# Kernel optimization log

Hardware: AMD Instinct MI355X
Metric: run time of the kernel (lower is better)

## Reference

```python
import jax, jax.numpy as jnp
import numpy as np

N = 8192
HIDDEN = 1024
PROJ = 128
T = 0.07
LN_EPS = 1e-12


def _neg_indices(n):
    # Static [n, n-2] index matrix: for row i, all j except j==i and the
    # paired sample j == (i + n//2) % n. Computed with numpy (n is static).
    half = n // 2
    idx = np.arange(n)
    mask = np.ones((n, n), dtype=bool)
    mask[idx, idx] = False
    mask[idx, (idx + half) % n] = False
    return np.nonzero(mask)[1].reshape(n, n - 2)


def setup_inputs() -> dict:
    key = jax.random.key(0)
    ks = jax.random.split(key, 3)
    scale = 1.0 / np.sqrt(HIDDEN)
    return {
        "x": jax.random.normal(ks[0], (N, HIDDEN), dtype=jnp.float32),
        "dense_w": jax.random.normal(ks[1], (HIDDEN, HIDDEN), dtype=jnp.float32) * scale,
        "dense_b": jnp.zeros((HIDDEN,), dtype=jnp.float32),
        "ln_gamma": jnp.ones((HIDDEN,), dtype=jnp.float32),
        "ln_beta": jnp.zeros((HIDDEN,), dtype=jnp.float32),
        "dec_w": jax.random.normal(ks[2], (HIDDEN, PROJ), dtype=jnp.float32) * scale,
        "dec_b": jnp.zeros((PROJ,), dtype=jnp.float32),
    }


def reference(x, dense_w, dense_b, ln_gamma, ln_beta, dec_w, dec_b):
    # dense -> gelu (exact, erf-based as in BERT) -> layernorm -> decoder
    h = x @ dense_w + dense_b
    h = jax.nn.gelu(h, approximate=False)
    mu = jnp.mean(h, axis=-1, keepdims=True)
    var = jnp.mean(jnp.square(h - mu), axis=-1, keepdims=True)
    h = (h - mu) * jax.lax.rsqrt(var + LN_EPS) * ln_gamma + ln_beta
    z = h @ dec_w + dec_b  # [N, 128]

    n = z.shape[0]
    half = n // 2
    # positive logit: dot(z_i, z_partner)
    l_pos = jnp.sum(z[:half] * z[half:], axis=-1)  # [N/2]
    l_pos = jnp.concatenate([l_pos, l_pos])[:, None]  # [N, 1]

    # full similarity matrix, then gather the N-2 negatives per row
    sims = z @ z.T  # [N, N]
    neg_idx = jnp.asarray(_neg_indices(n))  # static [N, N-2]
    l_neg = jnp.take_along_axis(sims, neg_idx, axis=1)  # [N, N-2]

    logits = jnp.concatenate([l_pos, l_neg], axis=1) / T  # [N, N-1]
    # CrossEntropyLoss with labels == 0
    loss = jnp.mean(jax.nn.logsumexp(logits, axis=-1) - logits[:, 0])
    return loss
```

## Files before the change

kernel.cpp:

```cpp
#include <hip/hip_runtime.h>
#include <math.h>
#include <stdint.h>

#define NN 8192
#define HID 1024
#define PROJ 128

constexpr float INV_T = 1.0f / 0.07f;
constexpr float LN_EPS = 1e-12f;
constexpr float CC = 14.285714285714286f * 1.4426950408889634f;

typedef __bf16 bf16x8 __attribute__((ext_vector_type(8)));
typedef float f32x4 __attribute__((ext_vector_type(4)));

#define EXP2(x) __builtin_amdgcn_exp2f(x)

#define GLD16(g, l)                                                     \
  __builtin_amdgcn_global_load_lds(                                     \
      (const __attribute__((address_space(1))) uint32_t*)(g),           \
      (__attribute__((address_space(3))) uint32_t*)(l), 16, 0, 0)

__device__ __forceinline__ uint16_t f2bf(float f) {
  union { float f; uint32_t u; } c; c.f = f;
  uint32_t r = (c.u + 0x7FFFu + ((c.u >> 16) & 1u)) >> 16;
  return (uint16_t)r;
}
__device__ __forceinline__ float bf2f(uint16_t u) {
  union { uint32_t u; float f; } c; c.u = ((uint32_t)u) << 16;
  return c.f;
}

__global__ __launch_bounds__(256) void k_conv(const float* __restrict__ in,
                                              uint16_t* __restrict__ out) {
  int i = (blockIdx.x * 256 + threadIdx.x) * 4;
  float4 v = *(const float4*)(in + i);
  ushort4 o;
  o.x = f2bf(v.x); o.y = f2bf(v.y); o.z = f2bf(v.z); o.w = f2bf(v.w);
  *(ushort4*)(out + i) = o;
}

__global__ __launch_bounds__(256) void k_transpose(const float* __restrict__ in,
                                                   uint16_t* __restrict__ out,
                                                   int R, int C) {
  __shared__ uint16_t t[32][33];
  const int cb = blockIdx.x * 32, rb = blockIdx.y * 32;
  const int tr = threadIdx.x >> 3, tc4 = (threadIdx.x & 7) * 4;
  float4 v = *(const float4*)(in + (size_t)(rb + tr) * C + cb + tc4);
  t[tc4 + 0][tr] = f2bf(v.x);
  t[tc4 + 1][tr] = f2bf(v.y);
  t[tc4 + 2][tr] = f2bf(v.z);
  t[tc4 + 3][tr] = f2bf(v.w);
  __syncthreads();
  const int oc = threadIdx.x >> 3, or4 = (threadIdx.x & 7) * 4;
  ushort4 o;
  o.x = t[oc][or4 + 0]; o.y = t[oc][or4 + 1];
  o.z = t[oc][or4 + 2]; o.w = t[oc][or4 + 3];
  *(ushort4*)(out + (size_t)(cb + oc) * R + rb + or4) = o;
}

__global__ __launch_bounds__(256) void k_gemm1(
    const uint16_t* __restrict__ Ab, const uint16_t* __restrict__ Bt,
    const float* __restrict__ bias, uint16_t* __restrict__ Hout) {
  __shared__ __align__(16) uint16_t As[128 * 32];
  __shared__ __align__(16) uint16_t Bs[128 * 32];
  const int tid = threadIdx.x;
  const int bn = blockIdx.x * 128, bm = blockIdx.y * 128;
  const int wave = tid >> 6, lane = tid & 63;
  const int wx = wave & 1, wy = wave >> 1;
  const int col = lane & 15, quad = lane >> 4;
  f32x4 acc[4][4] = {};
  const char* Abase = (const char*)Ab;
  const char* Bbase = (const char*)Bt;
  for (int k0 = 0; k0 < HID; k0 += 32) {
    __syncthreads();
#pragma unroll
    for (int l = 0; l < 2; ++l) {
      int off = tid * 16 + l * 4096;
      int row = off >> 6, inner = off & 63;
      GLD16(Abase + ((size_t)(bm + row) * HID + k0) * 2 + inner,
            (char*)As + off);
    }
#pragma unroll
    for (int l = 0; l < 2; ++l) {
      int off = tid * 16 + l * 4096;
      int row = off >> 6, inner = off & 63;
      GLD16(Bbase + ((size_t)(bn + row) * HID + k0) * 2 + inner,
            (char*)Bs + off);
    }
    __syncthreads();
    bf16x8 a[4], b[4];
#pragma unroll
    for (int mt = 0; mt < 4; ++mt)
      a[mt] = *(const bf16x8*)&As[(wy * 64 + mt * 16 + col) * 32 + quad * 8];
#pragma unroll
    for (int nt = 0; nt < 4; ++nt)
      b[nt] = *(const bf16x8*)&Bs[(wx * 64 + nt * 16 + col) * 32 + quad * 8];
#pragma unroll
    for (int mt = 0; mt < 4; ++mt)
#pragma unroll
      for (int nt = 0; nt < 4; ++nt)
        acc[mt][nt] = __builtin_amdgcn_mfma_f32_16x16x32_bf16(
            a[mt], b[nt], acc[mt][nt], 0, 0, 0);
  }
  const float is2 = 0.70710678118654752f;
#pragma unroll
  for (int nt = 0; nt < 4; ++nt) {
    int gj = bn + wx * 64 + nt * 16 + col;
    float bv = bias[gj];
#pragma unroll
    for (int mt = 0; mt < 4; ++mt) {
#pragma unroll
      for (int r = 0; r < 4; ++r) {
        int gi = bm + wy * 64 + mt * 16 + quad * 4 + r;
        float v = acc[mt][nt][r] + bv;
        float g = 0.5f * v * (1.0f + erff(v * is2));
        Hout[(size_t)gi * HID + gj] = f2bf(g);
      }
    }
  }
}

__global__ __launch_bounds__(256) void k_layernorm(
    uint16_t* __restrict__ Hm, const float* __restrict__ gamma,
    const float* __restrict__ beta) {
  const int row = blockIdx.x;
  const int tid = threadIdx.x;
  uint16_t* hr = Hm + (size_t)row * HID;
  ushort4 u = *(const ushort4*)(hr + tid * 4);
  float f0 = bf2f(u.x), f1 = bf2f(u.y), f2 = bf2f(u.z), f3 = bf2f(u.w);
  float sum = f0 + f1 + f2 + f3;
  float sq = f0 * f0 + f1 * f1 + f2 * f2 + f3 * f3;
#pragma unroll
  for (int off = 32; off > 0; off >>= 1) {
    sum += __shfl_down(sum, off);
    sq += __shfl_down(sq, off);
  }
  __shared__ float rs[4], rq[4];
  __shared__ float mu_s, rstd_s;
  const int wave = tid >> 6, lane = tid & 63;
  if (lane == 0) { rs[wave] = sum; rq[wave] = sq; }
  __syncthreads();
  if (tid == 0) {
    float s = rs[0] + rs[1] + rs[2] + rs[3];
    float q = rq[0] + rq[1] + rq[2] + rq[3];
    float mu = s * (1.0f / HID);
    float var = q * (1.0f / HID) - mu * mu;
    mu_s = mu;
    rstd_s = rsqrtf(var + LN_EPS);
  }
  __syncthreads();
  const float mu = mu_s, r = rstd_s;
  float4 g = *(const float4*)(gamma + tid * 4);
  float4 b = *(const float4*)(beta + tid * 4);
  ushort4 o;
  o.x = f2bf((f0 - mu) * r * g.x + b.x);
  o.y = f2bf((f1 - mu) * r * g.y + b.y);
  o.z = f2bf((f2 - mu) * r * g.z + b.z);
  o.w = f2bf((f3 - mu) * r * g.w + b.w);
  *(ushort4*)(hr + tid * 4) = o;
}

__global__ __launch_bounds__(256) void k_gemm2(
    const uint16_t* __restrict__ Hn, const uint16_t* __restrict__ Wt2,
    const float* __restrict__ bd, uint16_t* __restrict__ Z) {
  __shared__ __align__(16) uint16_t As2[64 * 32];
  __shared__ __align__(16) uint16_t Bs2[128 * 32];
  const int tid = threadIdx.x;
  const int bm = blockIdx.x * 64;
  const int wave = tid >> 6, lane = tid & 63;
  const int wx = wave & 1, wy = wave >> 1;
  const int col = lane & 15, quad = lane >> 4;
  f32x4 acc[2][4] = {};
  const char* Abase = (const char*)Hn;
  const char* Bbase = (const char*)Wt2;
  for (int k0 = 0; k0 < HID; k0 += 32) {
    __syncthreads();
    {
      int off = tid * 16;
      int row = off >> 6, inner = off & 63;
      GLD16(Abase + ((size_t)(bm + row) * HID + k0) * 2 + inner,
            (char*)As2 + off);
    }
#pragma unroll
    for (int l = 0; l < 2; ++l) {
      int off = tid * 16 + l * 4096;
      int row = off >> 6, inner = off & 63;
      GLD16(Bbase + ((size_t)row * HID + k0) * 2 + inner, (char*)Bs2 + off);
    }
    __syncthreads();
    bf16x8 a[2], b[4];
#pragma unroll
    for (int mt = 0; mt < 2; ++mt)
      a[mt] = *(const bf16x8*)&As2[(wy * 32 + mt * 16 + col) * 32 + quad * 8];
#pragma unroll
    for (int nt = 0; nt < 4; ++nt)
      b[nt] = *(const bf16x8*)&Bs2[(wx * 64 + nt * 16 + col) * 32 + quad * 8];
#pragma unroll
    for (int mt = 0; mt < 2; ++mt)
#pragma unroll
      for (int nt = 0; nt < 4; ++nt)
        acc[mt][nt] = __builtin_amdgcn_mfma_f32_16x16x32_bf16(
            a[mt], b[nt], acc[mt][nt], 0, 0, 0);
  }
#pragma unroll
  for (int nt = 0; nt < 4; ++nt) {
    int gj = wx * 64 + nt * 16 + col;
    float bv = bd[gj];
#pragma unroll
    for (int mt = 0; mt < 2; ++mt)
#pragma unroll
      for (int r = 0; r < 4; ++r) {
        int gi = bm + wy * 32 + mt * 16 + quad * 4 + r;
        Z[(size_t)gi * PROJ + gj] = f2bf(acc[mt][nt][r] + bv);
      }
  }
}

__device__ __forceinline__ void lse_update(float& m, float& s, float v0,
                                           float v1, float v2, float v3) {
  float lm = fmaxf(fmaxf(v0, v1), fmaxf(v2, v3));
  float mn = fmaxf(m, lm);
  float t = mn * CC;
  s = s * EXP2(m * CC - t) + EXP2(v0 * CC - t) + EXP2(v1 * CC - t) +
      EXP2(v2 * CC - t) + EXP2(v3 * CC - t);
  m = mn;
}

__global__ __launch_bounds__(256) void k_sim(const uint16_t* __restrict__ Z,
                                             float* __restrict__ m_part,
                                             float* __restrict__ s_part,
                                             float* __restrict__ pos_arr) {
  __shared__ __align__(16) uint16_t Zi[128 * 136];
  __shared__ __align__(16) uint16_t Zj[128 * 136];
  const int tid = threadIdx.x;
  const int bi = blockIdx.x * 128;
  const int chunk = blockIdx.y;
  const int wave = tid >> 6, lane = tid & 63;
  const int wx = wave & 1, wy = wave >> 1;
  const int col = lane & 15, quad = lane >> 4;

#pragma unroll
  for (int l = 0; l < 8; ++l) {
    int idx = tid + l * 256;
    int row = idx >> 4, kq = (idx & 15) * 8;
    *(uint4*)&Zi[row * 136 + kq] = *(const uint4*)(Z + (size_t)(bi + row) * PROJ + kq);
  }
  float mrow[16], srow[16];
#pragma unroll
  for (int i = 0; i < 16; ++i) { mrow[i] = -INFINITY; srow[i] = 0.f; }

  const int jbase = chunk * 1024;
  for (int t = 0; t < 8; ++t) {
    const int j0 = jbase + t * 128;
    __syncthreads();
#pragma unroll
    for (int l = 0; l < 8; ++l) {
      int idx = tid + l * 256;
      int row = idx >> 4, kq = (idx & 15) * 8;
      *(uint4*)&Zj[row * 136 + kq] =
          *(const uint4*)(Z + (size_t)(j0 + row) * PROJ + kq);
    }
    __syncthreads();
    f32x4 acc[4][4] = {};
#pragma unroll
    for (int kc = 0; kc < 4; ++kc) {
      bf16x8 a[4], b[4];
#pragma unroll
      for (int mt = 0; mt < 4; ++mt)
        a[mt] = *(const bf16x8*)&Zi[(wy * 64 + mt * 16 + col) * 136 +
                                    kc * 32 + quad * 8];
#pragma unroll
      for (int nt = 0; nt < 4; ++nt)
        b[nt] = *(const bf16x8*)&Zj[(wx * 64 + nt * 16 + col) * 136 +
                                    kc * 32 + quad * 8];
#pragma unroll
      for (int mt = 0; mt < 4; ++mt)
#pragma unroll
        for (int nt = 0; nt < 4; ++nt)
          acc[mt][nt] = __builtin_amdgcn_mfma_f32_16x16x32_bf16(
              a[mt], b[nt], acc[mt][nt], 0, 0, 0);
    }
    const bool is_diag = (j0 == bi);
    const bool is_pos = (j0 == ((bi + NN / 2) & (NN - 1)));
    if (!(is_diag || is_pos)) {
#pragma unroll
      for (int mt = 0; mt < 4; ++mt)
#pragma unroll
        for (int r = 0; r < 4; ++r)
          lse_update(mrow[mt * 4 + r], srow[mt * 4 + r], acc[mt][0][r],
                     acc[mt][1][r], acc[mt][2][r], acc[mt][3][r]);
    } else {
#pragma unroll
      for (int mt = 0; mt < 4; ++mt)
#pragma unroll
        for (int r = 0; r < 4; ++r) {
          int gi = bi + wy * 64 + mt * 16 + quad * 4 + r;
          int partner = (gi + NN / 2) & (NN - 1);
          float v[4];
#pragma unroll
          for (int nt = 0; nt < 4; ++nt) {
            int gj = j0 + wx * 64 + nt * 16 + col;
            float d = acc[mt][nt][r];
            if (is_pos && gj == partner) pos_arr[gi] = d;
            v[nt] = (is_diag && gj == gi) ? -INFINITY : d;
          }
          lse_update(mrow[mt * 4 + r], srow[mt * 4 + r], v[0], v[1], v[2],
                     v[3]);
        }
    }
  }
#pragma unroll
  for (int ri = 0; ri < 16; ++ri) {
#pragma unroll
    for (int off = 1; off < 16; off <<= 1) {
      float om = __shfl_xor(mrow[ri], off, 64);
      float os = __shfl_xor(srow[ri], off, 64);
      float mn = fmaxf(mrow[ri], om);
      float t = mn * CC;
      srow[ri] = srow[ri] * EXP2(mrow[ri] * CC - t) + os * EXP2(om * CC - t);
      mrow[ri] = mn;
    }
  }
  if (col == 0) {
    int p = chunk * 2 + wx;
#pragma unroll
    for (int ri = 0; ri < 16; ++ri) {
      int gi = bi + wy * 64 + (ri >> 2) * 16 + quad * 4 + (ri & 3);
      m_part[(size_t)p * NN + gi] = mrow[ri];
      s_part[(size_t)p * NN + gi] = srow[ri];
    }
  }
}

__global__ __launch_bounds__(256) void k_combine(
    const float* __restrict__ m_part, const float* __restrict__ s_part,
    const float* __restrict__ pos_arr, float* __restrict__ row_loss) {
  const int i = blockIdx.x * 256 + threadIdx.x;
  float M = -INFINITY;
#pragma unroll
  for (int p = 0; p < 16; ++p) M = fmaxf(M, m_part[(size_t)p * NN + i]);
  float S = 0.f;
  float t = M * CC;
#pragma unroll
  for (int p = 0; p < 16; ++p)
    S += s_part[(size_t)p * NN + i] * EXP2(m_part[(size_t)p * NN + i] * CC - t);
  row_loss[i] = (M - pos_arr[i]) * INV_T + logf(S);
}

__global__ __launch_bounds__(256) void k_final(
    const float* __restrict__ row_loss, float* __restrict__ out) {
  const int tid = threadIdx.x;
  float s = 0.f;
#pragma unroll
  for (int l = 0; l < 32; ++l) s += row_loss[tid + l * 256];
#pragma unroll
  for (int off = 32; off > 0; off >>= 1) s += __shfl_down(s, off);
  __shared__ float red[4];
  const int wave = tid >> 6, lane = tid & 63;
  if (lane == 0) red[wave] = s;
  __syncthreads();
  if (tid == 0) out[0] = (red[0] + red[1] + red[2] + red[3]) * (1.0f / NN);
}

extern "C" void kernel_launch(void* const* d_in, const int* in_sizes, int n_in,
                              void* d_out, int out_size, void* d_ws,
                              size_t ws_size, hipStream_t stream) {
  const float* x       = (const float*)d_in[0];
  const float* dense_w = (const float*)d_in[1];
  const float* dense_b = (const float*)d_in[2];
  const float* ln_g    = (const float*)d_in[3];
  const float* ln_b    = (const float*)d_in[4];
  const float* dec_w   = (const float*)d_in[5];
  const float* dec_b   = (const float*)d_in[6];
  float* out = (float*)d_out;
  char* ws = (char*)d_ws;
  uint16_t* xb = (uint16_t*)(ws);
  uint16_t* wt = (uint16_t*)(ws + 16777216);
  uint16_t* h  = (uint16_t*)(ws + 18874368);
  uint16_t* wt2     = (uint16_t*)(ws);
  uint16_t* z       = (uint16_t*)(ws + 262144);
  float*    m_part  = (float*)(ws + 2359296);
  float*    s_part  = (float*)(ws + 2883584);
  float*    pos_arr = (float*)(ws + 3407872);
  float*    row_loss= (float*)(ws + 3440640);

  k_conv<<<dim3(NN * HID / 1024), 256, 0, stream>>>(x, xb);
  k_transpose<<<dim3(32, 32), 256, 0, stream>>>(dense_w, wt, HID, HID);
  k_gemm1<<<dim3(HID / 128, NN / 128), 256, 0, stream>>>(xb, wt, dense_b, h);
  k_transpose<<<dim3(PROJ / 32, HID / 32), 256, 0, stream>>>(dec_w, wt2, HID,
                                                             PROJ);
  k_layernorm<<<dim3(NN), 256, 0, stream>>>(h, ln_g, ln_b);
  k_gemm2<<<dim3(NN / 64), 256, 0, stream>>>(h, wt2, dec_b, z);
  k_sim<<<dim3(NN / 128, 8), 256, 0, stream>>>(z, m_part, s_part, pos_arr);
  k_combine<<<dim3(NN / 256), 256, 0, stream>>>(m_part, s_part, pos_arr,
                                                row_loss);
  k_final<<<dim3(1), 256, 0, stream>>>(row_loss, out);
}
```

Measured before the change: 204.9 us.

## Shrink tiles in all GEMMs, tanh-approx GELU, register-resident Zi in sim kernel

Halves the M-tile of gemm1 (128→64), gemm2 (64→32) and the similarity kernel (128→64), and doubles the j-chunk count to 16. This raises block count and occupancy on a GPU with many CUs. The similarity kernel now keeps its row fragments in registers instead of LDS. The exact erf GELU is replaced with a tanh-form approximation built from exp2 and rcp, which is cheaper but deviates slightly from the erf reference. Smaller tiles lower data reuse per block, and the partial buffers and combine work double.

Measured after the change: 199.7 us. 1.03x faster.

```diff
diff --git a/kernel.cpp b/kernel.cpp
--- a/kernel.cpp
+++ b/kernel.cpp
@@ -28,6 +28,13 @@
 __device__ __forceinline__ float bf2f(uint16_t u) {
   union { uint32_t u; float f; } c; c.u = ((uint32_t)u) << 16;
   return c.f;
+}
+
+__device__ __forceinline__ float gelu_f(float v) {
+  float w = v * v;
+  float u = v * fmaf(w, 0.0356774081f, 0.7978845608f);
+  float e = EXP2(u * -2.8853900818f);
+  return v * __builtin_amdgcn_rcpf(1.0f + e);
 }
 
 __global__ __launch_bounds__(256) void k_conv(const float* __restrict__ in,
@@ -61,21 +68,20 @@
 __global__ __launch_bounds__(256) void k_gemm1(
     const uint16_t* __restrict__ Ab, const uint16_t* __restrict__ Bt,
     const float* __restrict__ bias, uint16_t* __restrict__ Hout) {
-  __shared__ __align__(16) uint16_t As[128 * 32];
+  __shared__ __align__(16) uint16_t As[64 * 32];
   __shared__ __align__(16) uint16_t Bs[128 * 32];
   const int tid = threadIdx.x;
-  const int bn = blockIdx.x * 128, bm = blockIdx.y * 128;
+  const int bn = blockIdx.x * 128, bm = blockIdx.y * 64;
   const int wave = tid >> 6, lane = tid & 63;
   const int wx = wave & 1, wy = wave >> 1;
   const int col = lane & 15, quad = lane >> 4;
-  f32x4 acc[4][4] = {};
+  f32x4 acc[2][4] = {};
   const char* Abase = (const char*)Ab;
   const char* Bbase = (const char*)Bt;
   for (int k0 = 0; k0 < HID; k0 += 32) {
     __syncthreads();
-#pragma unroll
-    for (int l = 0; l < 2; ++l) {
-      int off = tid * 16 + l * 4096;
+    {
+      int off = tid * 16;
       int row = off >> 6, inner = off & 63;
       GLD16(Abase + ((size_t)(bm + row) * HID + k0) * 2 + inner,
             (char*)As + off);
@@ -88,35 +94,31 @@
             (char*)Bs + off);
     }
     __syncthreads();
-    bf16x8 a[4], b[4];
-#pragma unroll
-    for (int mt = 0; mt < 4; ++mt)
-      a[mt] = *(const bf16x8*)&As[(wy * 64 + mt * 16 + col) * 32 + quad * 8];
+    bf16x8 a[2], b[4];
+#pragma unroll
+    for (int mt = 0; mt < 2; ++mt)
+      a[mt] = *(const bf16x8*)&As[(wy * 32 + mt * 16 + col) * 32 + quad * 8];
 #pragma unroll
     for (int nt = 0; nt < 4; ++nt)
       b[nt] = *(const bf16x8*)&Bs[(wx * 64 + nt * 16 + col) * 32 + quad * 8];
 #pragma unroll
-    for (int mt = 0; mt < 4; ++mt)
+    for (int mt = 0; mt < 2; ++mt)
 #pragma unroll
       for (int nt = 0; nt < 4; ++nt)
         acc[mt][nt] = __builtin_amdgcn_mfma_f32_16x16x32_bf16(
             a[mt], b[nt], acc[mt][nt], 0, 0, 0);
   }
-  const float is2 = 0.70710678118654752f;
 #pragma unroll
   for (int nt = 0; nt < 4; ++nt) {
     int gj = bn + wx * 64 + nt * 16 + col;
     float bv = bias[gj];
 #pragma unroll
-    for (int mt = 0; mt < 4; ++mt) {
+    for (int mt = 0; mt < 2; ++mt)
 #pragma unroll
       for (int r = 0; r < 4; ++r) {
-        int gi = bm + wy * 64 + mt * 16 + quad * 4 + r;
-        float v = acc[mt][nt][r] + bv;
-        float g = 0.5f * v * (1.0f + erff(v * is2));
-        Hout[(size_t)gi * HID + gj] = f2bf(g);
+        int gi = bm + wy * 32 + mt * 16 + quad * 4 + r;
+        Hout[(size_t)gi * HID + gj] = f2bf(gelu_f(acc[mt][nt][r] + bv));
       }
-    }
   }
 }
 
@@ -163,19 +165,19 @@
 __global__ __launch_bounds__(256) void k_gemm2(
     const uint16_t* __restrict__ Hn, const uint16_t* __restrict__ Wt2,
     const float* __restrict__ bd, uint16_t* __restrict__ Z) {
-  __shared__ __align__(16) uint16_t As2[64 * 32];
+  __shared__ __align__(16) uint16_t As2[32 * 32];
   __shared__ __align__(16) uint16_t Bs2[128 * 32];
   const int tid = threadIdx.x;
-  const int bm = blockIdx.x * 64;
+  const int bm = blockIdx.x * 32;
   const int wave = tid >> 6, lane = tid & 63;
   const int wx = wave & 1, wy = wave >> 1;
   const int col = lane & 15, quad = lane >> 4;
-  f32x4 acc[2][4] = {};
+  f32x4 acc[4] = {};
   const char* Abase = (const char*)Hn;
   const char* Bbase = (const char*)Wt2;
   for (int k0 = 0; k0 < HID; k0 += 32) {
     __syncthreads();
-    {
+    if (tid < 128) {
       int off = tid * 16;
       int row = off >> 6, inner = off & 63;
       GLD16(Abase + ((size_t)(bm + row) * HID + k0) * 2 + inner,
@@ -188,31 +190,22 @@
       GLD16(Bbase + ((size_t)row * HID + k0) * 2 + inner, (char*)Bs2 + off);
     }
     __syncthreads();
-    bf16x8 a[2], b[4];
-#pragma unroll
-    for (int mt = 0; mt < 2; ++mt)
-      a[mt] = *(const bf16x8*)&As2[(wy * 32 + mt * 16 + col) * 32 + quad * 8];
-#pragma unroll
-    for (int nt = 0; nt < 4; ++nt)
-      b[nt] = *(const bf16x8*)&Bs2[(wx * 64 + nt * 16 + col) * 32 + quad * 8];
-#pragma unroll
-    for (int mt = 0; mt < 2; ++mt)
-#pragma unroll
-      for (int nt = 0; nt < 4; ++nt)
-        acc[mt][nt] = __builtin_amdgcn_mfma_f32_16x16x32_bf16(
-            a[mt], b[nt], acc[mt][nt], 0, 0, 0);
+    bf16x8 a = *(const bf16x8*)&As2[(wy * 16 + col) * 32 + quad * 8];
+#pragma unroll
+    for (int nt = 0; nt < 4; ++nt) {
+      bf16x8 b = *(const bf16x8*)&Bs2[(wx * 64 + nt * 16 + col) * 32 + quad * 8];
+      acc[nt] = __builtin_amdgcn_mfma_f32_16x16x32_bf16(a, b, acc[nt], 0, 0, 0);
+    }
   }
 #pragma unroll
   for (int nt = 0; nt < 4; ++nt) {
     int gj = wx * 64 + nt * 16 + col;
     float bv = bd[gj];
 #pragma unroll
-    for (int mt = 0; mt < 2; ++mt)
-#pragma unroll
-      for (int r = 0; r < 4; ++r) {
-        int gi = bm + wy * 32 + mt * 16 + quad * 4 + r;
-        Z[(size_t)gi * PROJ + gj] = f2bf(acc[mt][nt][r] + bv);
-      }
+    for (int r = 0; r < 4; ++r) {
+      int gi = bm + wy * 16 + quad * 4 + r;
+      Z[(size_t)gi * PROJ + gj] = f2bf(acc[nt][r] + bv);
+    }
   }
 }
 
@@ -230,27 +223,28 @@
                                              float* __restrict__ m_part,
                                              float* __restrict__ s_part,
                                              float* __restrict__ pos_arr) {
-  __shared__ __align__(16) uint16_t Zi[128 * 136];
   __shared__ __align__(16) uint16_t Zj[128 * 136];
   const int tid = threadIdx.x;
-  const int bi = blockIdx.x * 128;
+  const int bi = blockIdx.x * 64;
   const int chunk = blockIdx.y;
   const int wave = tid >> 6, lane = tid & 63;
   const int wx = wave & 1, wy = wave >> 1;
   const int col = lane & 15, quad = lane >> 4;
 
-#pragma unroll
-  for (int l = 0; l < 8; ++l) {
-    int idx = tid + l * 256;
-    int row = idx >> 4, kq = (idx & 15) * 8;
-    *(uint4*)&Zi[row * 136 + kq] = *(const uint4*)(Z + (size_t)(bi + row) * PROJ + kq);
-  }
-  float mrow[16], srow[16];
-#pragma unroll
-  for (int i = 0; i < 16; ++i) { mrow[i] = -INFINITY; srow[i] = 0.f; }
-
-  const int jbase = chunk * 1024;
-  for (int t = 0; t < 8; ++t) {
+  bf16x8 afr[2][4];
+#pragma unroll
+  for (int mt = 0; mt < 2; ++mt)
+#pragma unroll
+    for (int kc = 0; kc < 4; ++kc)
+      afr[mt][kc] = *(const bf16x8*)(Z +
+          (size_t)(bi + wy * 32 + mt * 16 + col) * PROJ + kc * 32 + quad * 8);
+
+  float mrow[8], srow[8];
+#pragma unroll
+  for (int i = 0; i < 8; ++i) { mrow[i] = -INFINITY; srow[i] = 0.f; }
+
+  const int jbase = chunk * 512;
+  for (int t = 0; t < 4; ++t) {
     const int j0 = jbase + t * 128;
     __syncthreads();
 #pragma unroll
@@ -261,40 +255,36 @@
           *(const uint4*)(Z + (size_t)(j0 + row) * PROJ + kq);
     }
     __syncthreads();
-    f32x4 acc[4][4] = {};
+    f32x4 acc[2][4] = {};
 #pragma unroll
     for (int kc = 0; kc < 4; ++kc) {
-      bf16x8 a[4], b[4];
-#pragma unroll
-      for (int mt = 0; mt < 4; ++mt)
-        a[mt] = *(const bf16x8*)&Zi[(wy * 64 + mt * 16 + col) * 136 +
-                                    kc * 32 + quad * 8];
+      bf16x8 b[4];
 #pragma unroll
       for (int nt = 0; nt < 4; ++nt)
         b[nt] = *(const bf16x8*)&Zj[(wx * 64 + nt * 16 + col) * 136 +
                                     kc * 32 + quad * 8];
 #pragma unroll
-      for (int mt = 0; mt < 4; ++mt)
+      for (int mt = 0; mt < 2; ++mt)
 #pragma unroll
         for (int nt = 0; nt < 4; ++nt)
           acc[mt][nt] = __builtin_amdgcn_mfma_f32_16x16x32_bf16(
-              a[mt], b[nt], acc[mt][nt], 0, 0, 0);
-    }
-    const bool is_diag = (j0 == bi);
-    const bool is_pos = (j0 == ((bi + NN / 2) & (NN - 1)));
+              afr[mt][kc], b[nt], acc[mt][nt], 0, 0, 0);
+    }
+    const bool is_diag = (j0 == (bi & ~127));
+    const bool is_pos = (j0 == (((bi + NN / 2) & (NN - 1)) & ~127));
     if (!(is_diag || is_pos)) {
 #pragma unroll
-      for (int mt = 0; mt < 4; ++mt)
+      for (int mt = 0; mt < 2; ++mt)
 #pragma unroll
         for (int r = 0; r < 4; ++r)
           lse_update(mrow[mt * 4 + r], srow[mt * 4 + r], acc[mt][0][r],
                      acc[mt][1][r], acc[mt][2][r], acc[mt][3][r]);
     } else {
 #pragma unroll
-      for (int mt = 0; mt < 4; ++mt)
+      for (int mt = 0; mt < 2; ++mt)
 #pragma unroll
         for (int r = 0; r < 4; ++r) {
-          int gi = bi + wy * 64 + mt * 16 + quad * 4 + r;
+          int gi = bi + wy * 32 + mt * 16 + quad * 4 + r;
           int partner = (gi + NN / 2) & (NN - 1);
           float v[4];
 #pragma unroll
@@ -310,7 +300,7 @@
     }
   }
 #pragma unroll
-  for (int ri = 0; ri < 16; ++ri) {
+  for (int ri = 0; ri < 8; ++ri) {
 #pragma unroll
     for (int off = 1; off < 16; off <<= 1) {
       float om = __shfl_xor(mrow[ri], off, 64);
@@ -324,8 +314,8 @@
   if (col == 0) {
     int p = chunk * 2 + wx;
 #pragma unroll
-    for (int ri = 0; ri < 16; ++ri) {
-      int gi = bi + wy * 64 + (ri >> 2) * 16 + quad * 4 + (ri & 3);
+    for (int ri = 0; ri < 8; ++ri) {
+      int gi = bi + wy * 32 + (ri >> 2) * 16 + quad * 4 + (ri & 3);
       m_part[(size_t)p * NN + gi] = mrow[ri];
       s_part[(size_t)p * NN + gi] = srow[ri];
     }
@@ -338,11 +328,11 @@
   const int i = blockIdx.x * 256 + threadIdx.x;
   float M = -INFINITY;
 #pragma unroll
-  for (int p = 0; p < 16; ++p) M = fmaxf(M, m_part[(size_t)p * NN + i]);
+  for (int p = 0; p < 32; ++p) M = fmaxf(M, m_part[(size_t)p * NN + i]);
   float S = 0.f;
   float t = M * CC;
 #pragma unroll
-  for (int p = 0; p < 16; ++p)
+  for (int p = 0; p < 32; ++p)
     S += s_part[(size_t)p * NN + i] * EXP2(m_part[(size_t)p * NN + i] * CC - t);
   row_loss[i] = (M - pos_arr[i]) * INV_T + logf(S);
 }
@@ -380,18 +370,18 @@
   uint16_t* wt2     = (uint16_t*)(ws);
   uint16_t* z       = (uint16_t*)(ws + 262144);
   float*    m_part  = (float*)(ws + 2359296);
-  float*    s_part  = (float*)(ws + 2883584);
-  float*    pos_arr = (float*)(ws + 3407872);
-  float*    row_loss= (float*)(ws + 3440640);
+  float*    s_part  = (float*)(ws + 3407872);
+  float*    pos_arr = (float*)(ws + 4456448);
+  float*    row_loss= (float*)(ws + 4489216);
 
   k_conv<<<dim3(NN * HID / 1024), 256, 0, stream>>>(x, xb);
   k_transpose<<<dim3(32, 32), 256, 0, stream>>>(dense_w, wt, HID, HID);
-  k_gemm1<<<dim3(HID / 128, NN / 128), 256, 0, stream>>>(xb, wt, dense_b, h);
+  k_gemm1<<<dim3(HID / 128, NN / 64), 256, 0, stream>>>(xb, wt, dense_b, h);
   k_transpose<<<dim3(PROJ / 32, HID / 32), 256, 0, stream>>>(dec_w, wt2, HID,
                                                              PROJ);
   k_layernorm<<<dim3(NN), 256, 0, stream>>>(h, ln_g, ln_b);
-  k_gemm2<<<dim3(NN / 64), 256, 0, stream>>>(h, wt2, dec_b, z);
-  k_sim<<<dim3(NN / 128, 8), 256, 0, stream>>>(z, m_part, s_part, pos_arr);
+  k_gemm2<<<dim3(NN / 32), 256, 0, stream>>>(h, wt2, dec_b, z);
+  k_sim<<<dim3(NN / 64, 16), 256, 0, stream>>>(z, m_part, s_part, pos_arr);
   k_combine<<<dim3(NN / 256), 256, 0, stream>>>(m_part, s_part, pos_arr,
                                                 row_loss);
   k_final<<<dim3(1), 256, 0, stream>>>(row_loss, out);
```
